# Performance work log

Hardware: AMD Instinct MI355X
Metric: run time of the kernel (lower is better)

The kernel has to match this reference:

```python
import jax, jax.numpy as jnp
import numpy as np

N_NODES = 100000
N_EDGES = 3200000
D_IN, D_HID, D_OUT = 128, 64, 64


def setup_inputs() -> dict:
    key = jax.random.key(0)
    ks = jax.random.split(key, 8)
    x = jax.random.normal(ks[0], (N_NODES, D_IN), dtype=jnp.float32)
    edge_index = jax.random.randint(ks[1], (2, N_EDGES), 0, N_NODES, dtype=jnp.int32)
    # Glorot-ish init for GCN weights, zero bias (PyG default)
    def w(k, fi, fo):
        s = (6.0 / (fi + fo)) ** 0.5
        return jax.random.uniform(k, (fi, fo), jnp.float32, -s, s)
    return {
        "x": x,
        "edge_index": edge_index,
        "W1": w(ks[2], D_IN, D_HID), "b1": jnp.zeros((D_HID,), jnp.float32),
        "W2": w(ks[3], D_HID, D_HID), "b2": jnp.zeros((D_HID,), jnp.float32),
        "W3": w(ks[4], D_HID, D_OUT), "b3": jnp.zeros((D_OUT,), jnp.float32),
    }


def _gcn_layer(x, W, b, src, dst, norm, num_nodes):
    # GCNConv: out[i] = sum_{j->i} norm_ji * (x W)[j] + b   (self-loops included in src/dst)
    h = x @ W                                   # [N, F_out] small GEMM
    msg = h[src] * norm[:, None]                # [E+N, F_out] gather
    out = jax.ops.segment_sum(msg, dst, num_segments=num_nodes)  # scatter-add
    return out + b


def reference(x, edge_index, W1, b1, W2, b2, W3, b3):
    n = x.shape[0]
    loop = jnp.arange(n, dtype=edge_index.dtype)
    src = jnp.concatenate([edge_index[0], loop])  # add self-loops (GCN default)
    dst = jnp.concatenate([edge_index[1], loop])
    # symmetric normalization: deg^{-1/2}[src] * deg^{-1/2}[dst]
    deg = jax.ops.segment_sum(jnp.ones_like(dst, dtype=x.dtype), dst, num_segments=n)
    dinv = jnp.where(deg > 0, jax.lax.rsqrt(deg), 0.0)
    norm = dinv[src] * dinv[dst]

    h = jax.nn.relu(_gcn_layer(x, W1, b1, src, dst, norm, n))
    h = jax.nn.relu(_gcn_layer(h, W2, b2, src, dst, norm, n))
    out = _gcn_layer(h, W3, b3, src, dst, norm, n)
    return out
```

## Files before the change

### kernel.cpp

```cpp
#include <hip/hip_runtime.h>

static inline size_t align256(size_t x) { return (x + 255) & ~(size_t)255; }


__global__ __launch_bounds__(1024) void bucket_hist_kernel(const int* __restrict__ dst,
                                                           int* __restrict__ bcnt,
                                                           int e, int nb, int tile) {
    __shared__ int hist[512];
    const int t = threadIdx.x;
    const int lo = blockIdx.x * tile;
    const int hi = min(lo + tile, e);
    for (int i = t; i < 512; i += 1024) hist[i] = 0;
    __syncthreads();
    for (int i = lo + t; i < hi; i += 1024) atomicAdd(&hist[dst[i] >> 8], 1);
    __syncthreads();
    for (int i = t; i < nb; i += 1024) {
        int c = hist[i];
        if (c) atomicAdd(&bcnt[i], c);
    }
}

__global__ __launch_bounds__(512) void bucket_scan_kernel(const int* __restrict__ bcnt,
                                                          int* __restrict__ bstart,
                                                          int* __restrict__ cursor, int nb) {
    __shared__ int lds[512];
    const int t = threadIdx.x;
    int v = (t < nb) ? bcnt[t] : 0;
    lds[t] = v;
    __syncthreads();
    for (int off = 1; off < 512; off <<= 1) {
        int add = (t >= off) ? lds[t - off] : 0;
        __syncthreads();
        lds[t] += add;
        __syncthreads();
    }
    if (t < nb) {
        int excl = lds[t] - v;
        bstart[t] = excl;
        cursor[t] = excl;
        if (t == nb - 1) bstart[nb] = lds[t];
    }
}

__global__ __launch_bounds__(1024) void partition_place_kernel(const int* __restrict__ src,
                                                               const int* __restrict__ dst,
                                                               int* __restrict__ cursor,
                                                               unsigned int* __restrict__ part,
                                                               int e, int nb, int tile) {
    __shared__ int hist[512];
    __shared__ int base[512];
    const int t = threadIdx.x;
    const int lo = blockIdx.x * tile;
    const int hi = min(lo + tile, e);
    for (int i = t; i < nb; i += 1024) hist[i] = 0;
    __syncthreads();
    for (int i = lo + t; i < hi; i += 1024) atomicAdd(&hist[dst[i] >> 8], 1);
    __syncthreads();
    for (int i = t; i < nb; i += 1024) {
        int c = hist[i];
        base[i] = c ? atomicAdd(&cursor[i], c) : 0;
        hist[i] = 0;
    }
    __syncthreads();
    for (int i = lo + t; i < hi; i += 1024) {
        int s = src[i], d = dst[i];
        int b = d >> 8;
        int p = base[b] + atomicAdd(&hist[b], 1);
        part[p] = ((unsigned int)s << 8) | (unsigned int)(d & 255);
    }
}

__global__ __launch_bounds__(512) void csr_build_place_kernel(const unsigned int* __restrict__ part,
                                                              const int* __restrict__ bstart,
                                                              int* __restrict__ row_ptr,
                                                              float* __restrict__ dinv,
                                                              int* __restrict__ col, int n) {
    __shared__ int cnt[256];
    __shared__ int scan[256];
    __shared__ int cur[256];
    const int t = threadIdx.x;
    const int node0 = blockIdx.x << 8;
    const int e0 = bstart[blockIdx.x];
    const int e1 = bstart[blockIdx.x + 1];
    if (t < 256) cnt[t] = 0;
    __syncthreads();
    for (int i = e0 + t; i < e1; i += 512) atomicAdd(&cnt[part[i] & 255u], 1);
    __syncthreads();
    const int v = (t < 256) ? cnt[t] : 0;
    if (t < 256) scan[t] = v;
    __syncthreads();
    for (int off = 1; off < 256; off <<= 1) {
        int add = (t >= off && t < 256) ? scan[t - off] : 0;
        __syncthreads();
        if (t < 256) scan[t] += add;
        __syncthreads();
    }
    if (t < 256) {
        const int node = node0 + t;
        const int excl = e0 + scan[t] - v;
        cur[t] = excl;
        if (node < n) {
            row_ptr[node] = excl;
            dinv[node] = rsqrtf((float)(v + 1));
            if (node == n - 1) row_ptr[n] = e1;
        }
    }
    __syncthreads();
    for (int i = e0 + t; i < e1; i += 512) {
        unsigned int sd = part[i];
        int p = atomicAdd(&cur[sd & 255u], 1);
        col[p] = (int)(sd >> 8);
    }
}


__device__ __forceinline__ unsigned int bf16rne(float f) {
    unsigned int u = __float_as_uint(f);
    return (u + 0x7fffu + ((u >> 16) & 1u)) >> 16;
}
__device__ __forceinline__ unsigned int bf16pack(float a, float b) {
    return bf16rne(a) | (bf16rne(b) << 16);
}

template<int K>
__global__ __launch_bounds__(256) void gemm_scale(const float* __restrict__ A,
                                                  const float* __restrict__ W,
                                                  const float* __restrict__ dinv,
                                                  unsigned int* __restrict__ gout, int n) {
    constexpr int KC = 64;
    constexpr int ROWS = 128;
    constexpr int LDX = KC + 4;
    __shared__ float xs[ROWS * LDX];
    __shared__ float ws[KC * 64];
    const int t = threadIdx.x;
    const int r0 = blockIdx.x * ROWS;
    const int rt = t >> 3;
    const int c4 = (t & 7) * 2;

    float acc[4][8];
#pragma unroll
    for (int a = 0; a < 4; ++a)
#pragma unroll
        for (int b = 0; b < 8; ++b) acc[a][b] = 0.f;

    for (int kc = 0; kc < K; kc += KC) {
        {
            const float4* Wg = (const float4*)(W + kc * 64);
            for (int i = t; i < KC * 16; i += 256) ((float4*)ws)[i] = Wg[i];
        }
        {
            const int jr = t >> 4;
            const int j = t & 15;
            for (int r = jr; r < ROWS; r += 16) {
                const int gr = r0 + r;
                float4 v = make_float4(0.f, 0.f, 0.f, 0.f);
                if (gr < n) v = ((const float4*)A)[(size_t)gr * (K / 4) + (kc >> 2) + j];
                *(float4*)&xs[r * LDX + j * 4] = v;
            }
        }
        __syncthreads();
#pragma unroll 4
        for (int k = 0; k < KC; ++k) {
            const float4 w0 = ((const float4*)ws)[k * 16 + c4];
            const float4 w1 = ((const float4*)ws)[k * 16 + c4 + 1];
#pragma unroll
            for (int rr = 0; rr < 4; ++rr) {
                const float xv = xs[(rt + rr * 32) * LDX + k];
                acc[rr][0] = fmaf(xv, w0.x, acc[rr][0]);
                acc[rr][1] = fmaf(xv, w0.y, acc[rr][1]);
                acc[rr][2] = fmaf(xv, w0.z, acc[rr][2]);
                acc[rr][3] = fmaf(xv, w0.w, acc[rr][3]);
                acc[rr][4] = fmaf(xv, w1.x, acc[rr][4]);
                acc[rr][5] = fmaf(xv, w1.y, acc[rr][5]);
                acc[rr][6] = fmaf(xv, w1.z, acc[rr][6]);
                acc[rr][7] = fmaf(xv, w1.w, acc[rr][7]);
            }
        }
        __syncthreads();
    }
#pragma unroll
    for (int rr = 0; rr < 4; ++rr) {
        const int gr = r0 + rt + rr * 32;
        if (gr < n) {
            const float d = dinv[gr];
            uint4 o;
            o.x = bf16pack(acc[rr][0] * d, acc[rr][1] * d);
            o.y = bf16pack(acc[rr][2] * d, acc[rr][3] * d);
            o.z = bf16pack(acc[rr][4] * d, acc[rr][5] * d);
            o.w = bf16pack(acc[rr][6] * d, acc[rr][7] * d);
            ((uint4*)gout)[(size_t)gr * 8 + (t & 7)] = o;
        }
    }
}


__device__ __forceinline__ void bf4add(float4& a, const uint2 v) {
    a.x += __uint_as_float(v.x << 16);
    a.y += __uint_as_float(v.x & 0xffff0000u);
    a.z += __uint_as_float(v.y << 16);
    a.w += __uint_as_float(v.y & 0xffff0000u);
}

__global__ __launch_bounds__(256) void aggregate_kernel(const uint2* __restrict__ g,
                                                        const int* __restrict__ row_ptr,
                                                        const int* __restrict__ col,
                                                        const float* __restrict__ dinv,
                                                        const float* __restrict__ bias,
                                                        float4* __restrict__ out,
                                                        int n, int do_relu) {
    const int t = threadIdx.x;
    const int node = blockIdx.x * 16 + (t >> 4);
    const int fc = t & 15;
    if (node >= n) return;
    float4 acc = make_float4(0.f, 0.f, 0.f, 0.f);
    bf4add(acc, g[(size_t)node * 16 + fc]);
    const int e0 = row_ptr[node];
    const int e1 = row_ptr[node + 1];
    int e = e0;
    for (; e + 8 <= e1; e += 8) {
        int s[8];
#pragma unroll
        for (int j = 0; j < 8; ++j) s[j] = col[e + j];
        uint2 v[8];
#pragma unroll
        for (int j = 0; j < 8; ++j) v[j] = g[(size_t)s[j] * 16 + fc];
#pragma unroll
        for (int j = 0; j < 8; ++j) bf4add(acc, v[j]);
    }
    for (; e < e1; ++e) bf4add(acc, g[(size_t)col[e] * 16 + fc]);
    const float d = dinv[node];
    const float4 b = ((const float4*)bias)[fc];
    float4 o;
    o.x = fmaf(acc.x, d, b.x);
    o.y = fmaf(acc.y, d, b.y);
    o.z = fmaf(acc.z, d, b.z);
    o.w = fmaf(acc.w, d, b.w);
    if (do_relu) {
        o.x = fmaxf(o.x, 0.f); o.y = fmaxf(o.y, 0.f);
        o.z = fmaxf(o.z, 0.f); o.w = fmaxf(o.w, 0.f);
    }
    out[(size_t)node * 16 + fc] = o;
}


extern "C" void kernel_launch(void* const* d_in, const int* in_sizes, int n_in,
                              void* d_out, int out_size, void* d_ws, size_t ws_size,
                              hipStream_t stream) {
    const float* x  = (const float*)d_in[0];
    const int*   ei = (const int*)d_in[1];
    const float* W1 = (const float*)d_in[2];
    const float* b1 = (const float*)d_in[3];
    const float* W2 = (const float*)d_in[4];
    const float* b2 = (const float*)d_in[5];
    const float* W3 = (const float*)d_in[6];
    const float* b3 = (const float*)d_in[7];
    float* out = (float*)d_out;

    const int n = in_sizes[0] / 128;
    const int e = in_sizes[1] / 2;
    const int* srcv = ei;
    const int* dstv = ei + e;

    char* ws = (char*)d_ws;
    size_t off = 0;
    float* dinv   = (float*)(ws + off); off = align256(off + (size_t)n * 4);
    int* row_ptr  = (int*)(ws + off);   off = align256(off + (size_t)(n + 1) * 4);
    int* bcnt     = (int*)(ws + off);   off = align256(off + 1024 * 4);
    int* bstart   = (int*)(ws + off);   off = align256(off + 1024 * 4);
    int* cursor   = (int*)(ws + off);   off = align256(off + 1024 * 4);
    int* col      = (int*)(ws + off);   off = align256(off + (size_t)e * 4);
    unsigned int* gbuf = (unsigned int*)(ws + off); off = align256(off + (size_t)n * 64 * 2);
    unsigned int* part = gbuf;
    (void)ws_size; (void)n_in; (void)out_size;

    const int nbkt = (n + 255) >> 8;

    hipMemsetAsync(bcnt, 0, 1024 * 4, stream);
    const int G = 400;
    const int tile = (e + G - 1) / G;
    bucket_hist_kernel<<<G, 1024, 0, stream>>>(dstv, bcnt, e, nbkt, tile);
    bucket_scan_kernel<<<1, 512, 0, stream>>>(bcnt, bstart, cursor, nbkt);
    partition_place_kernel<<<G, 1024, 0, stream>>>(srcv, dstv, cursor, part, e, nbkt, tile);
    csr_build_place_kernel<<<nbkt, 512, 0, stream>>>(part, bstart, row_ptr, dinv, col, n);

    const int gemm_grid = (n + 127) / 128;
    const int agg_grid = (n + 15) / 16;

    gemm_scale<128><<<gemm_grid, 256, 0, stream>>>(x, W1, dinv, gbuf, n);
    aggregate_kernel<<<agg_grid, 256, 0, stream>>>((const uint2*)gbuf, row_ptr, col,
                                                   dinv, b1, (float4*)out, n, 1);
    gemm_scale<64><<<gemm_grid, 256, 0, stream>>>(out, W2, dinv, gbuf, n);
    aggregate_kernel<<<agg_grid, 256, 0, stream>>>((const uint2*)gbuf, row_ptr, col,
                                                   dinv, b2, (float4*)out, n, 1);
    gemm_scale<64><<<gemm_grid, 256, 0, stream>>>(out, W3, dinv, gbuf, n);
    aggregate_kernel<<<agg_grid, 256, 0, stream>>>((const uint2*)gbuf, row_ptr, col,
                                                   dinv, b3, (float4*)out, n, 0);
}
```

Before: 435.1 us.

## Fuse aggregation with next layer's GEMM and widen CSR build blocks

Layers 1 and 2 now aggregate neighbor features, apply bias and ReLU, then multiply by the next weight matrix in shared memory and write bf16 scaled output in one kernel. This removes two standalone GEMM launches and the fp32 round trip of the hidden activations through global memory. A second ping-pong bf16 buffer is added, and each block loads the whole 64x64 weight into shared memory, which adds per-block setup and LDS pressure. The CSR placement kernel is also moved to 1024 threads per block.

```diff
diff --git a/kernel.cpp b/kernel.cpp
--- a/kernel.cpp
+++ b/kernel.cpp
@@ -70,11 +70,11 @@
     }
 }
 
-__global__ __launch_bounds__(512) void csr_build_place_kernel(const unsigned int* __restrict__ part,
-                                                              const int* __restrict__ bstart,
-                                                              int* __restrict__ row_ptr,
-                                                              float* __restrict__ dinv,
-                                                              int* __restrict__ col, int n) {
+__global__ __launch_bounds__(1024) void csr_build_place_kernel(const unsigned int* __restrict__ part,
+                                                               const int* __restrict__ bstart,
+                                                               int* __restrict__ row_ptr,
+                                                               float* __restrict__ dinv,
+                                                               int* __restrict__ col, int n) {
     __shared__ int cnt[256];
     __shared__ int scan[256];
     __shared__ int cur[256];
@@ -84,7 +84,7 @@
     const int e1 = bstart[blockIdx.x + 1];
     if (t < 256) cnt[t] = 0;
     __syncthreads();
-    for (int i = e0 + t; i < e1; i += 512) atomicAdd(&cnt[part[i] & 255u], 1);
+    for (int i = e0 + t; i < e1; i += 1024) atomicAdd(&cnt[part[i] & 255u], 1);
     __syncthreads();
     const int v = (t < 256) ? cnt[t] : 0;
     if (t < 256) scan[t] = v;
@@ -106,7 +106,7 @@
         }
     }
     __syncthreads();
-    for (int i = e0 + t; i < e1; i += 512) {
+    for (int i = e0 + t; i < e1; i += 1024) {
         unsigned int sd = part[i];
         int p = atomicAdd(&cur[sd & 255u], 1);
         col[p] = (int)(sd >> 8);
@@ -121,6 +121,13 @@
 __device__ __forceinline__ unsigned int bf16pack(float a, float b) {
     return bf16rne(a) | (bf16rne(b) << 16);
 }
+__device__ __forceinline__ void bf4add(float4& a, const uint2 v) {
+    a.x += __uint_as_float(v.x << 16);
+    a.y += __uint_as_float(v.x & 0xffff0000u);
+    a.z += __uint_as_float(v.y << 16);
+    a.w += __uint_as_float(v.y & 0xffff0000u);
+}
+
 
 template<int K>
 __global__ __launch_bounds__(256) void gemm_scale(const float* __restrict__ A,
@@ -194,12 +201,70 @@
 }
 
 
-__device__ __forceinline__ void bf4add(float4& a, const uint2 v) {
-    a.x += __uint_as_float(v.x << 16);
-    a.y += __uint_as_float(v.x & 0xffff0000u);
-    a.z += __uint_as_float(v.y << 16);
-    a.w += __uint_as_float(v.y & 0xffff0000u);
-}
+__global__ __launch_bounds__(256) void fused_agg_gemm_kernel(const uint2* __restrict__ g,
+                                                             const int* __restrict__ row_ptr,
+                                                             const int* __restrict__ col,
+                                                             const float* __restrict__ dinv,
+                                                             const float* __restrict__ bias,
+                                                             const float* __restrict__ W,
+                                                             unsigned int* __restrict__ gout,
+                                                             int n) {
+    __shared__ float ws[64 * 64];
+    __shared__ float hs[16 * 68];
+    const int t = threadIdx.x;
+    const int r = t >> 4;
+    const int fc = t & 15;
+    const int node = blockIdx.x * 16 + r;
+    const bool valid = node < n;
+
+    for (int i = t; i < 1024; i += 256) ((float4*)ws)[i] = ((const float4*)W)[i];
+
+    float4 acc = make_float4(0.f, 0.f, 0.f, 0.f);
+    if (valid) {
+        bf4add(acc, g[(size_t)node * 16 + fc]);
+        const int e0 = row_ptr[node];
+        const int e1 = row_ptr[node + 1];
+        int e = e0;
+        for (; e + 8 <= e1; e += 8) {
+            int s[8];
+#pragma unroll
+            for (int j = 0; j < 8; ++j) s[j] = col[e + j];
+            uint2 v[8];
+#pragma unroll
+            for (int j = 0; j < 8; ++j) v[j] = g[(size_t)s[j] * 16 + fc];
+#pragma unroll
+            for (int j = 0; j < 8; ++j) bf4add(acc, v[j]);
+        }
+        for (; e < e1; ++e) bf4add(acc, g[(size_t)col[e] * 16 + fc]);
+        const float d = dinv[node];
+        const float4 b = ((const float4*)bias)[fc];
+        acc.x = fmaxf(fmaf(acc.x, d, b.x), 0.f);
+        acc.y = fmaxf(fmaf(acc.y, d, b.y), 0.f);
+        acc.z = fmaxf(fmaf(acc.z, d, b.z), 0.f);
+        acc.w = fmaxf(fmaf(acc.w, d, b.w), 0.f);
+    }
+    *(float4*)&hs[r * 68 + fc * 4] = acc;
+    __syncthreads();
+
+    float a0 = 0.f, a1 = 0.f, a2 = 0.f, a3 = 0.f;
+#pragma unroll 8
+    for (int k = 0; k < 64; ++k) {
+        const float hv = hs[r * 68 + k];
+        const float4 wv = ((const float4*)ws)[k * 16 + fc];
+        a0 = fmaf(hv, wv.x, a0);
+        a1 = fmaf(hv, wv.y, a1);
+        a2 = fmaf(hv, wv.z, a2);
+        a3 = fmaf(hv, wv.w, a3);
+    }
+    if (valid) {
+        const float d2 = dinv[node];
+        uint2 o;
+        o.x = bf16pack(a0 * d2, a1 * d2);
+        o.y = bf16pack(a2 * d2, a3 * d2);
+        ((uint2*)gout)[(size_t)node * 16 + fc] = o;
+    }
+}
+
 
 __global__ __launch_bounds__(256) void aggregate_kernel(const uint2* __restrict__ g,
                                                         const int* __restrict__ row_ptr,
@@ -207,7 +272,7 @@
                                                         const float* __restrict__ dinv,
                                                         const float* __restrict__ bias,
                                                         float4* __restrict__ out,
-                                                        int n, int do_relu) {
+                                                        int n) {
     const int t = threadIdx.x;
     const int node = blockIdx.x * 16 + (t >> 4);
     const int fc = t & 15;
@@ -235,10 +300,6 @@
     o.y = fmaf(acc.y, d, b.y);
     o.z = fmaf(acc.z, d, b.z);
     o.w = fmaf(acc.w, d, b.w);
-    if (do_relu) {
-        o.x = fmaxf(o.x, 0.f); o.y = fmaxf(o.y, 0.f);
-        o.z = fmaxf(o.z, 0.f); o.w = fmaxf(o.w, 0.f);
-    }
     out[(size_t)node * 16 + fc] = o;
 }
 
@@ -269,8 +330,9 @@
     int* bstart   = (int*)(ws + off);   off = align256(off + 1024 * 4);
     int* cursor   = (int*)(ws + off);   off = align256(off + 1024 * 4);
     int* col      = (int*)(ws + off);   off = align256(off + (size_t)e * 4);
-    unsigned int* gbuf = (unsigned int*)(ws + off); off = align256(off + (size_t)n * 64 * 2);
-    unsigned int* part = gbuf;
+    unsigned int* gbuf  = (unsigned int*)(ws + off); off = align256(off + (size_t)n * 64 * 2);
+    unsigned int* gbuf2 = (unsigned int*)(ws + off); off = align256(off + (size_t)n * 64 * 2);
+    unsigned int* part  = gbuf;
     (void)ws_size; (void)n_in; (void)out_size;
 
     const int nbkt = (n + 255) >> 8;
@@ -281,18 +343,16 @@
     bucket_hist_kernel<<<G, 1024, 0, stream>>>(dstv, bcnt, e, nbkt, tile);
     bucket_scan_kernel<<<1, 512, 0, stream>>>(bcnt, bstart, cursor, nbkt);
     partition_place_kernel<<<G, 1024, 0, stream>>>(srcv, dstv, cursor, part, e, nbkt, tile);
-    csr_build_place_kernel<<<nbkt, 512, 0, stream>>>(part, bstart, row_ptr, dinv, col, n);
+    csr_build_place_kernel<<<nbkt, 1024, 0, stream>>>(part, bstart, row_ptr, dinv, col, n);
 
     const int gemm_grid = (n + 127) / 128;
     const int agg_grid = (n + 15) / 16;
 
     gemm_scale<128><<<gemm_grid, 256, 0, stream>>>(x, W1, dinv, gbuf, n);
+    fused_agg_gemm_kernel<<<agg_grid, 256, 0, stream>>>((const uint2*)gbuf, row_ptr, col,
+                                                        dinv, b1, W2, gbuf2, n);
+    fused_agg_gemm_kernel<<<agg_grid, 256, 0, stream>>>((const uint2*)gbuf2, row_ptr, col,
+                                                        dinv, b2, W3, gbuf, n);
     aggregate_kernel<<<agg_grid, 256, 0, stream>>>((const uint2*)gbuf, row_ptr, col,
-                                                   dinv, b1, (float4*)out, n, 1);
-    gemm_scale<64><<<gemm_grid, 256, 0, stream>>>(out, W2, dinv, gbuf, n);
-    aggregate_kernel<<<agg_grid, 256, 0, stream>>>((const uint2*)gbuf, row_ptr, col,
-                                                   dinv, b2, (float4*)out, n, 1);
-    gemm_scale<64><<<gemm_grid, 256, 0, stream>>>(out, W3, dinv, gbuf, n);
-    aggregate_kernel<<<agg_grid, 256, 0, stream>>>((const uint2*)gbuf, row_ptr, col,
-                                                   dinv, b3, (float4*)out, n, 0);
-}
+                                                   dinv, b3, (float4*)out, n);
+}
```

Measured after the change: 413.0 us. -5.1%, faster.
